# Kernel optimization log

Measured on AMD Instinct MI355X. Metric: run time of the kernel, lower is better.

The kernel has to match this reference:

```python
import jax, jax.numpy as jnp
import numpy as np

ALPHA = 0.2  # LeakyReLU negative slope


def setup_inputs() -> dict:
    key = jax.random.key(0)
    k1, k2, k3, k4 = jax.random.split(key, 4)
    B, N, F_in, F_out = 16, 2048, 64, 64
    h = jax.random.normal(k1, (B, N, F_in), dtype=jnp.float32)
    bias_mat = jnp.zeros((B, N, N), dtype=jnp.float32)
    # xavier_uniform with gain=1.414
    def xavier(k, shape, gain=1.414):
        fan_in, fan_out = shape[0], shape[1]
        bound = gain * np.sqrt(6.0 / (fan_in + fan_out))
        return jax.random.uniform(k, shape, jnp.float32, -bound, bound)
    W = xavier(k2, (F_in, F_out))
    a1 = xavier(k3, (F_out, 1))
    a2 = xavier(k4, (F_out, 1))
    return {"h": h, "bias_mat": bias_mat, "W": W, "a1": a1, "a2": a2}


def reference(h, bias_mat, W, a1, a2):
    # h: [B, N, F_in]; W: [F_in, F_out]
    Wh = jnp.einsum("bnf,fo->bno", h, W)            # [B, N, F_out]
    Wh1 = jnp.einsum("bno,oi->bni", Wh, a1)          # [B, N, 1]
    Wh2 = jnp.einsum("bno,oi->bni", Wh, a2)          # [B, N, 1]
    e = Wh1 + jnp.swapaxes(Wh2, 1, 2)                # [B, N, N] additive scores
    e = jax.nn.leaky_relu(e, negative_slope=ALPHA) + bias_mat
    attention = jax.nn.softmax(e, axis=2)            # row-wise over neighbors
    h_prime = jnp.einsum("bnm,bmo->bno", attention, Wh)
    return h_prime
```

## Files before the change

kernel.cpp:

```cpp
#include <hip/hip_runtime.h>
#include <hip/hip_bf16.h>
#include <cstdint>
#include <cstddef>

#define ALPHA 0.2f
#define LOG2E 1.4426950408889634f

using f32x4 = __attribute__((ext_vector_type(4))) float;
using s16x8 = __attribute__((ext_vector_type(8))) short;

typedef __attribute__((address_space(3))) unsigned lds_u32;
typedef __attribute__((address_space(1))) const unsigned glb_u32;

__device__ __forceinline__ unsigned f2bf(float f) {
  unsigned u = __float_as_uint(f);
  u = (u + 0x7fffu + ((u >> 16) & 1u)) >> 16;
  return u;
}

#define FENCE asm volatile("" ::: "memory")

__global__ __launch_bounds__(256) void k1_proj(
    const float* __restrict__ h, const float* __restrict__ W,
    const float* __restrict__ a1, const float* __restrict__ a2,
    unsigned short* __restrict__ whT, float* __restrict__ s1,
    float* __restrict__ s2) {
  __shared__ __align__(16) float h_lds[64 * 64];
  __shared__ __align__(16) float W_lds[64 * 64];
  __shared__ __align__(16) unsigned short t_lds[64 * 64];

  const int t = threadIdx.x;
  const int c = t & 63;
  const int w = t >> 6;
  const int row0 = blockIdx.x * 64;

  const float4* hg = (const float4*)(h + (size_t)row0 * 64);
  #pragma unroll
  for (int r = 0; r < 4; ++r) {
    ((float4*)h_lds)[t + r * 256] = hg[t + r * 256];
    ((float4*)W_lds)[t + r * 256] = ((const float4*)W)[t + r * 256];
  }
  const float a1v = a1[c];
  const float a2v = a2[c];
  __syncthreads();

  float acc[16];
  #pragma unroll
  for (int r = 0; r < 16; ++r) acc[r] = 0.0f;

  #pragma unroll 1
  for (int kc = 0; kc < 16; ++kc) {
    const float w0 = W_lds[(kc * 4 + 0) * 64 + c];
    const float w1 = W_lds[(kc * 4 + 1) * 64 + c];
    const float w2 = W_lds[(kc * 4 + 2) * 64 + c];
    const float w3 = W_lds[(kc * 4 + 3) * 64 + c];
    #pragma unroll
    for (int r = 0; r < 16; ++r) {
      const float4 hv = *(const float4*)(h_lds + (w * 16 + r) * 64 + kc * 4);
      acc[r] = fmaf(hv.x, w0, acc[r]);
      acc[r] = fmaf(hv.y, w1, acc[r]);
      acc[r] = fmaf(hv.z, w2, acc[r]);
      acc[r] = fmaf(hv.w, w3, acc[r]);
    }
  }

  #pragma unroll 1
  for (int r = 0; r < 16; ++r) {
    float v1 = acc[r] * a1v;
    float v2 = acc[r] * a2v;
    #pragma unroll
    for (int s = 1; s < 64; s <<= 1) {
      v1 += __shfl_xor(v1, s, 64);
      v2 += __shfl_xor(v2, s, 64);
    }
    if (c == 0) {
      s1[row0 + w * 16 + r] = v1;
      s2[row0 + w * 16 + r] = v2;
    }
  }

  #pragma unroll
  for (int hh = 0; hh < 2; ++hh) {
    uint4 pk;
    pk.x = f2bf(acc[hh * 8 + 0]) | (f2bf(acc[hh * 8 + 1]) << 16);
    pk.y = f2bf(acc[hh * 8 + 2]) | (f2bf(acc[hh * 8 + 3]) << 16);
    pk.z = f2bf(acc[hh * 8 + 4]) | (f2bf(acc[hh * 8 + 5]) << 16);
    pk.w = f2bf(acc[hh * 8 + 6]) | (f2bf(acc[hh * 8 + 7]) << 16);
    const int off = c * 128 + ((w * 32 + hh * 16) ^ ((c & 7) << 4));
    *(uint4*)((char*)t_lds + off) = pk;
  }
  __syncthreads();

  const int b = row0 >> 11;
  const int n0 = row0 & 2047;
  #pragma unroll
  for (int q = 0; q < 2; ++q) {
    const int chunk = q * 256 + t;
    const int cc = chunk >> 3;
    const int w8 = (chunk & 7) * 16;
    const uint4 v =
        *(const uint4*)((const char*)t_lds + cc * 128 + (w8 ^ ((cc & 7) << 4)));
    *(uint4*)((char*)whT + ((size_t)(b * 64 + cc) * 2048 + n0) * 2 + w8) = v;
  }
}

__global__ __launch_bounds__(256, 2) void k2_attn(
    const float* __restrict__ bias, const unsigned short* __restrict__ whT,
    const float* __restrict__ s1g, const float* __restrict__ s2g,
    float* __restrict__ out) {
  __shared__ __align__(16) unsigned short wbuf[4][4096];
  __shared__ __align__(16) float s2_lds[2048];

  const int t = threadIdx.x;
  const int lane = t & 63;
  const int w = t >> 6;
  const int arow = lane & 15;
  const int kgrp = lane >> 4;
  const int b = blockIdx.x >> 5;
  const int i0 = (blockIdx.x & 31) * 64;
  const int gi = i0 + w * 16 + arow;

  const float s1v = s1g[b * 2048 + gi];

  #pragma unroll
  for (int q = 0; q < 2; ++q)
    ((float4*)s2_lds)[t + q * 256] =
        ((const float4*)(s2g + b * 2048))[t + q * 256];
  __syncthreads();

  const char* whT_b = (const char*)whT + (size_t)b * 64 * 2048 * 2;
  const float* bias_p = bias + ((size_t)b * 2048 + gi) * 2048 + kgrp * 8;

  const int src_swz = ((lane & 7) * 16) ^ ((lane >> 3) << 4);
  const char* gsrc0 = whT_b + (size_t)(lane >> 3) * 4096 + src_swz;

  auto whT_gll = [&](int jt) {
    char* dst = (char*)wbuf + (jt & 3) * 8192;
    #pragma unroll
    for (int q = 0; q < 2; ++q) {
      const int chunk = w * 2 + q;
      __builtin_amdgcn_global_load_lds(
          (glb_u32*)(gsrc0 + (size_t)chunk * 8 * 4096 + jt * 128),
          (lds_u32*)(dst + chunk * 1024), 16, 0, 0);
    }
  };
  auto bias_load = [&](f32x4 (&dst)[4], int jt) {
    const float* p = bias_p + jt * 64;
    dst[0] = *(const f32x4*)(p);
    dst[1] = *(const f32x4*)(p + 4);
    dst[2] = *(const f32x4*)(p + 32);
    dst[3] = *(const f32x4*)(p + 36);
  };

  f32x4 acc[4];
  #pragma unroll
  for (int ct = 0; ct < 4; ++ct) acc[ct] = (f32x4){0.f, 0.f, 0.f, 0.f};
  float l = 0.0f;

  f32x4 biasA[4], biasB[4];
  bias_load(biasA, 0);
  FENCE;
  whT_gll(0);
  whT_gll(1);
  FENCE;
  bias_load(biasB, 1);
  FENCE;

  auto body = [&](int jt, f32x4 (&bcur)[4]) {
    if (jt + 2 < 32) whT_gll(jt + 2);
    FENCE;

    float ps = 0.0f;
    s16x8 afrag[2];
    #pragma unroll
    for (int f = 0; f < 2; ++f) {
      const f32x4 sa = *(const f32x4*)(s2_lds + jt * 64 + f * 32 + kgrp * 8);
      const f32x4 sb =
          *(const f32x4*)(s2_lds + jt * 64 + f * 32 + kgrp * 8 + 4);
      const f32x4 ba = bcur[f * 2 + 0];
      const f32x4 bb = bcur[f * 2 + 1];
      #pragma unroll
      for (int e = 0; e < 4; ++e) {
        float x = s1v + sa[e];
        x = fmaxf(x, ALPHA * x);
        const float p = exp2f((x + ba[e]) * LOG2E);
        ps += p;
        float y = s1v + sb[e];
        y = fmaxf(y, ALPHA * y);
        const float q = exp2f((y + bb[e]) * LOG2E);
        ps += q;
        afrag[f][e] = (short)f2bf(p);
        afrag[f][e + 4] = (short)f2bf(q);
      }
    }
    l += ps;

    if (jt + 2 < 32) bias_load(bcur, jt + 2);
    FENCE;

    asm volatile("s_waitcnt vmcnt(12)" ::: "memory");
    asm volatile("s_barrier" ::: "memory");

    const char* mybuf = (const char*)wbuf + (jt & 3) * 8192;
    #pragma unroll
    for (int ct = 0; ct < 4; ++ct) {
      const int cc = ct * 16 + arow;
      #pragma unroll
      for (int f = 0; f < 2; ++f) {
        const s16x8 bfrag = *(const s16x8*)(
            mybuf + cc * 128 + ((f * 64 + kgrp * 16) ^ ((cc & 7) << 4)));
        asm("s_nop 1\n\t"
            "v_mfma_f32_16x16x32_bf16 %0, %1, %2, %0"
            : "+v"(acc[ct])
            : "v"(afrag[f]), "v"(bfrag));
      }
    }
  };

  #pragma unroll 1
  for (int jt = 0; jt < 32; jt += 2) {
    body(jt + 0, biasA);
    body(jt + 1, biasB);
  }

  asm volatile("s_nop 7\n\ts_nop 7" ::: "memory");

  l += __shfl_xor(l, 16, 64);
  l += __shfl_xor(l, 32, 64);
  const float linv = 1.0f / l;
  #pragma unroll
  for (int r = 0; r < 4; ++r) {
    const float li = __shfl(linv, kgrp * 4 + r, 64);
    float* op = out + ((size_t)b * 2048 + i0 + w * 16 + kgrp * 4 + r) * 64;
    #pragma unroll
    for (int ct = 0; ct < 4; ++ct) op[ct * 16 + arow] = acc[ct][r] * li;
  }
}

extern "C" void kernel_launch(void* const* d_in, const int* in_sizes, int n_in,
                              void* d_out, int out_size, void* d_ws,
                              size_t ws_size, hipStream_t stream) {
  const float* h = (const float*)d_in[0];
  const float* bias = (const float*)d_in[1];
  const float* W = (const float*)d_in[2];
  const float* a1 = (const float*)d_in[3];
  const float* a2 = (const float*)d_in[4];
  float* out = (float*)d_out;

  char* ws = (char*)d_ws;
  unsigned short* whT = (unsigned short*)ws;
  float* s1 = (float*)(ws + 4 * 1024 * 1024);
  float* s2 = (float*)(ws + 4 * 1024 * 1024 + 128 * 1024);

  k1_proj<<<dim3(512), dim3(256), 0, stream>>>(h, W, a1, a2, whT, s1, s2);
  k2_attn<<<dim3(512), dim3(256), 0, stream>>>(bias, whT, s1, s2, out);
}
```

Baseline: 76.82 us.

## Register-tile k1 projection as 4x4 per thread and reduce scores via LDS

The projection kernel now gives each thread a 4-row by 4-column output tile instead of a 16-row by 1-column strip. The h tile is stored in LDS with an XOR swizzle, and W is read as float4 vectors, so each LDS load feeds more FMAs. The a1/a2 dot products use a partial in-thread sum, two cross-lane shuffles and a small LDS reduction across waves, replacing the 6-step full-wave shuffle reduction per row. This mainly targets the small k1 kernel, whose share of total time next to k2 is limited.

Measured after the change: 68.05 us, median of 2. 1.13x faster.

```diff
diff --git a/kernel.cpp b/kernel.cpp
--- a/kernel.cpp
+++ b/kernel.cpp
@@ -25,69 +25,83 @@
     const float* __restrict__ a1, const float* __restrict__ a2,
     unsigned short* __restrict__ whT, float* __restrict__ s1,
     float* __restrict__ s2) {
-  __shared__ __align__(16) float h_lds[64 * 64];
+  __shared__ __align__(16) char h_lds[64 * 256];
   __shared__ __align__(16) float W_lds[64 * 64];
   __shared__ __align__(16) unsigned short t_lds[64 * 64];
+  __shared__ float red[4][64][2];
 
   const int t = threadIdx.x;
-  const int c = t & 63;
+  const int l = t & 63;
   const int w = t >> 6;
+  const int rq = l & 15;
+  const int cq = w * 4 + (l >> 4);
+  const int c0 = cq * 4;
   const int row0 = blockIdx.x * 64;
 
   const float4* hg = (const float4*)(h + (size_t)row0 * 64);
   #pragma unroll
   for (int r = 0; r < 4; ++r) {
-    ((float4*)h_lds)[t + r * 256] = hg[t + r * 256];
-    ((float4*)W_lds)[t + r * 256] = ((const float4*)W)[t + r * 256];
-  }
-  const float a1v = a1[c];
-  const float a2v = a2[c];
+    const int f = t + r * 256;
+    const int n = f >> 4, ch = f & 15;
+    *(float4*)(h_lds + n * 256 + ((ch * 16) ^ (((n >> 2) & 7) << 4))) = hg[f];
+    ((float4*)W_lds)[f] = ((const float4*)W)[f];
+  }
+  const f32x4 a1v = *(const f32x4*)(a1 + c0);
+  const f32x4 a2v = *(const f32x4*)(a2 + c0);
   __syncthreads();
 
-  float acc[16];
-  #pragma unroll
-  for (int r = 0; r < 16; ++r) acc[r] = 0.0f;
+  f32x4 acc[4];
+  #pragma unroll
+  for (int i = 0; i < 4; ++i) acc[i] = (f32x4){0.f, 0.f, 0.f, 0.f};
 
   #pragma unroll 1
   for (int kc = 0; kc < 16; ++kc) {
-    const float w0 = W_lds[(kc * 4 + 0) * 64 + c];
-    const float w1 = W_lds[(kc * 4 + 1) * 64 + c];
-    const float w2 = W_lds[(kc * 4 + 2) * 64 + c];
-    const float w3 = W_lds[(kc * 4 + 3) * 64 + c];
-    #pragma unroll
-    for (int r = 0; r < 16; ++r) {
-      const float4 hv = *(const float4*)(h_lds + (w * 16 + r) * 64 + kc * 4);
-      acc[r] = fmaf(hv.x, w0, acc[r]);
-      acc[r] = fmaf(hv.y, w1, acc[r]);
-      acc[r] = fmaf(hv.z, w2, acc[r]);
-      acc[r] = fmaf(hv.w, w3, acc[r]);
-    }
-  }
-
-  #pragma unroll 1
-  for (int r = 0; r < 16; ++r) {
-    float v1 = acc[r] * a1v;
-    float v2 = acc[r] * a2v;
-    #pragma unroll
-    for (int s = 1; s < 64; s <<= 1) {
-      v1 += __shfl_xor(v1, s, 64);
-      v2 += __shfl_xor(v2, s, 64);
-    }
-    if (c == 0) {
-      s1[row0 + w * 16 + r] = v1;
-      s2[row0 + w * 16 + r] = v2;
-    }
-  }
-
-  #pragma unroll
-  for (int hh = 0; hh < 2; ++hh) {
-    uint4 pk;
-    pk.x = f2bf(acc[hh * 8 + 0]) | (f2bf(acc[hh * 8 + 1]) << 16);
-    pk.y = f2bf(acc[hh * 8 + 2]) | (f2bf(acc[hh * 8 + 3]) << 16);
-    pk.z = f2bf(acc[hh * 8 + 4]) | (f2bf(acc[hh * 8 + 5]) << 16);
-    pk.w = f2bf(acc[hh * 8 + 6]) | (f2bf(acc[hh * 8 + 7]) << 16);
-    const int off = c * 128 + ((w * 32 + hh * 16) ^ ((c & 7) << 4));
-    *(uint4*)((char*)t_lds + off) = pk;
+    f32x4 wv[4];
+    #pragma unroll
+    for (int kk = 0; kk < 4; ++kk)
+      wv[kk] = *(const f32x4*)(W_lds + (kc * 4 + kk) * 64 + c0);
+    #pragma unroll
+    for (int i = 0; i < 4; ++i) {
+      const int n = rq * 4 + i;
+      const f32x4 hv = *(const f32x4*)(
+          h_lds + n * 256 + ((kc * 16) ^ (((n >> 2) & 7) << 4)));
+      #pragma unroll
+      for (int j = 0; j < 4; ++j) {
+        acc[i][j] = fmaf(hv[0], wv[0][j], acc[i][j]);
+        acc[i][j] = fmaf(hv[1], wv[1][j], acc[i][j]);
+        acc[i][j] = fmaf(hv[2], wv[2][j], acc[i][j]);
+        acc[i][j] = fmaf(hv[3], wv[3][j], acc[i][j]);
+      }
+    }
+  }
+
+  float p1[4], p2[4];
+  #pragma unroll
+  for (int i = 0; i < 4; ++i) {
+    p1[i] = acc[i][0] * a1v[0] + acc[i][1] * a1v[1] + acc[i][2] * a1v[2] +
+            acc[i][3] * a1v[3];
+    p2[i] = acc[i][0] * a2v[0] + acc[i][1] * a2v[1] + acc[i][2] * a2v[2] +
+            acc[i][3] * a2v[3];
+    p1[i] += __shfl_xor(p1[i], 16, 64);
+    p1[i] += __shfl_xor(p1[i], 32, 64);
+    p2[i] += __shfl_xor(p2[i], 16, 64);
+    p2[i] += __shfl_xor(p2[i], 32, 64);
+  }
+  if (l < 16) {
+    #pragma unroll
+    for (int i = 0; i < 4; ++i) {
+      red[w][rq * 4 + i][0] = p1[i];
+      red[w][rq * 4 + i][1] = p2[i];
+    }
+  }
+
+  #pragma unroll
+  for (int j = 0; j < 4; ++j) {
+    const int c = c0 + j;
+    uint2 u;
+    u.x = f2bf(acc[0][j]) | (f2bf(acc[1][j]) << 16);
+    u.y = f2bf(acc[2][j]) | (f2bf(acc[3][j]) << 16);
+    *(uint2*)((char*)t_lds + c * 128 + ((rq * 8) ^ ((c & 7) << 4))) = u;
   }
   __syncthreads();
 
@@ -101,6 +115,15 @@
     const uint4 v =
         *(const uint4*)((const char*)t_lds + cc * 128 + (w8 ^ ((cc & 7) << 4)));
     *(uint4*)((char*)whT + ((size_t)(b * 64 + cc) * 2048 + n0) * 2 + w8) = v;
+  }
+  if (t < 128) {
+    const int n = t >> 1, v = t & 1;
+    const float s =
+        red[0][n][v] + red[1][n][v] + red[2][n][v] + red[3][n][v];
+    if (v == 0)
+      s1[row0 + n] = s;
+    else
+      s2[row0 + n] = s;
   }
 }
 
```
